# Optimization experiments

Measured on AMD Instinct MI355X. Metric: run time of the kernel, lower is better.

The kernel has to match this reference:

```python
import jax, jax.numpy as jnp
from jax import lax
import numpy as np

B, T, I, H, L, C = 64, 512, 128, 256, 2, 3


def _lstm_layer(x, W_ih, W_hh, b_ih, b_hh):
    # x: [B, T, in_dim]; W_ih: [4H, in_dim]; W_hh: [4H, H]
    # PyTorch gate order: i, f, g, o
    gates_x = jnp.einsum('bti,gi->btg', x, W_ih) + b_ih + b_hh  # [B, T, 4H]
    h0 = jnp.zeros((x.shape[0], W_hh.shape[1]), x.dtype)
    c0 = h0

    def step(carry, gx):
        h, c = carry
        g = gx + h @ W_hh.T  # [B, 4H]
        i, f, gg, o = jnp.split(g, 4, axis=-1)
        i = jax.nn.sigmoid(i)
        f = jax.nn.sigmoid(f)
        gg = jnp.tanh(gg)
        o = jax.nn.sigmoid(o)
        c = f * c + i * gg
        h = o * jnp.tanh(c)
        return (h, c), h

    _, hs = lax.scan(step, (h0, c0), jnp.swapaxes(gates_x, 0, 1))  # [T, B, H]
    return jnp.swapaxes(hs, 0, 1)  # [B, T, H]


def setup_inputs() -> dict:
    key = jax.random.key(0)
    ks = jax.random.split(key, 12)
    s = 1.0 / np.sqrt(H)
    u = lambda k, shape: jax.random.uniform(k, shape, jnp.float32, -s, s)
    return {
        'x': jax.random.normal(ks[0], (B, T, I), jnp.float32),
        'W_ih_0': u(ks[1], (4 * H, I)),
        'W_hh_0': u(ks[2], (4 * H, H)),
        'b_ih_0': u(ks[3], (4 * H,)),
        'b_hh_0': u(ks[4], (4 * H,)),
        'W_ih_1': u(ks[5], (4 * H, H)),
        'W_hh_1': u(ks[6], (4 * H, H)),
        'b_ih_1': u(ks[7], (4 * H,)),
        'b_hh_1': u(ks[8], (4 * H,)),
        'fc_w': u(ks[9], (C, H)),
        'fc_b': u(ks[10], (C,)),
    }


def reference(x, W_ih_0, W_hh_0, b_ih_0, b_hh_0, W_ih_1, W_hh_1, b_ih_1, b_hh_1, fc_w, fc_b):
    h = _lstm_layer(x, W_ih_0, W_hh_0, b_ih_0, b_hh_0)
    h = _lstm_layer(h, W_ih_1, W_hh_1, b_ih_1, b_hh_1)
    last = h[:, -1, :]                      # [B, H]
    logits = last @ fc_w.T + fc_b           # [B, C]
    return jax.nn.softmax(logits, axis=1)
```

## Files before the change

### kernel.cpp

```cpp
#include <hip/hip_runtime.h>
#include <cstdint>
#include <cstddef>

typedef _Float16 half2_t __attribute__((ext_vector_type(2)));
typedef _Float16 half8_t __attribute__((ext_vector_type(8)));
typedef float f32x4 __attribute__((ext_vector_type(4)));

static __device__ __forceinline__ float fdot2(half2_t a, half2_t b, float c) {
    return __builtin_amdgcn_fdot2(a, b, c, false);
}
static __device__ __forceinline__ half2_t h2(unsigned int u) {
    return __builtin_bit_cast(half2_t, u);
}
static __device__ __forceinline__ float sigm(float x) {
    return 1.f / (1.f + __expf(-x));
}
static __device__ __forceinline__ float tanh_fast(float x) {
    float ax = fabsf(x);
    float e = __expf(2.f * ax);
    float r = 1.f - 2.f / (e + 1.f);
    return copysignf(r, x);
}

__global__ __launch_bounds__(256) void prep_whh(const float* __restrict__ Whh,
                                                const float* __restrict__ bih,
                                                const float* __restrict__ bhh,
                                                uint4* __restrict__ Wp,
                                                float* __restrict__ bias) {
    int n = blockIdx.x * 256 + threadIdx.x;
    if (n < 1024) bias[n] = bih[n] + bhh[n];
    int p = n >> 9;
    int idx = n & 511;
    int qq = idx >> 8, jj = idx & 255;
    int g = p >> 4, u = p & 15;
    int row = g * 256 + jj;
    int kb = qq * 128 + u * 8;
    union { uint4 u4; _Float16 h[8]; } cv;
#pragma unroll
    for (int i = 0; i < 8; ++i) cv.h[i] = (_Float16)Whh[row * 256 + kb + i];
    Wp[p * 512 + idx] = cv.u4;
}

__global__ __launch_bounds__(256) void cvt_f16(const float* __restrict__ in,
                                               _Float16* __restrict__ out, int n4) {
    int i = blockIdx.x * 256 + threadIdx.x;
    if (i < n4) {
        float4 v = ((const float4*)in)[i];
        union { ushort4 u; _Float16 h[4]; } cv;
        cv.h[0] = (_Float16)v.x; cv.h[1] = (_Float16)v.y;
        cv.h[2] = (_Float16)v.z; cv.h[3] = (_Float16)v.w;
        ((ushort4*)out)[i] = cv.u;
    }
}

__global__ __launch_bounds__(256) void gemm_mfma(const _Float16* __restrict__ A,
                                                 const _Float16* __restrict__ Bw,
                                                 const float* __restrict__ bias,
                                                 float* __restrict__ Cmat, int K) {
    __shared__ _Float16 As[64][72];
    __shared__ _Float16 Bs[64][72];
    const int tid = threadIdx.x;
    const int wave = tid >> 6, lane = tid & 63;
    const int quad = lane >> 4, l16 = lane & 15;
    const int m0 = blockIdx.x * 64, n0 = blockIdx.y * 64;
    const int sr = tid >> 2;
    const int sc = (tid & 3) * 16;

    f32x4 acc[4] = {};

    for (int k0 = 0; k0 < K; k0 += 64) {
        const uint4 a0v = *(const uint4*)(A + (size_t)(m0 + sr) * K + k0 + sc);
        const uint4 a1v = *(const uint4*)(A + (size_t)(m0 + sr) * K + k0 + sc + 8);
        const uint4 b0v = *(const uint4*)(Bw + (size_t)(n0 + sr) * K + k0 + sc);
        const uint4 b1v = *(const uint4*)(Bw + (size_t)(n0 + sr) * K + k0 + sc + 8);
        __syncthreads();
        *(uint4*)&As[sr][sc] = a0v;
        *(uint4*)&As[sr][sc + 8] = a1v;
        *(uint4*)&Bs[sr][sc] = b0v;
        *(uint4*)&Bs[sr][sc + 8] = b1v;
        __syncthreads();
#pragma unroll
        for (int kc = 0; kc < 64; kc += 32) {
            half8_t af = *(const half8_t*)&As[wave * 16 + l16][kc + quad * 8];
#pragma unroll
            for (int nb = 0; nb < 4; ++nb) {
                half8_t bf = *(const half8_t*)&Bs[nb * 16 + l16][kc + quad * 8];
                acc[nb] = __builtin_amdgcn_mfma_f32_16x16x32_f16(af, bf, acc[nb], 0, 0, 0);
            }
        }
    }
#pragma unroll
    for (int nb = 0; nb < 4; ++nb) {
#pragma unroll
        for (int i = 0; i < 4; ++i) {
            int row = m0 + wave * 16 + quad * 4 + i;
            int col = n0 + nb * 16 + l16;
            Cmat[(size_t)row * 1024 + col] = acc[nb][i] + bias[col];
        }
    }
}

__global__ __launch_bounds__(512, 2)
void lstm_scan(const float* __restrict__ gx,
               const uint4* __restrict__ Wp,
               _Float16* __restrict__ h_out,
               int store_all) {
    const int b = blockIdx.x;
    const int tid = threadIdx.x;
    const int q = tid >> 8;
    const int j = tid & 255;
    const int l = tid & 63;

    __shared__ uint4 wlds[16 * 512];
    __shared__ f32x4 pex[512] __attribute__((aligned(16)));
    __shared__ _Float16 hbuf[2][256] __attribute__((aligned(16)));
    __shared__ _Float16 hist[8][256] __attribute__((aligned(16)));

#pragma unroll
    for (int p = 0; p < 16; ++p) wlds[p * 512 + tid] = Wp[(48 + p) * 512 + tid];
    uint4 wreg[48];
#pragma unroll
    for (int p = 0; p < 48; ++p) wreg[p] = Wp[p * 512 + tid];

    if (tid < 256) hbuf[0][tid] = (_Float16)0.f;
    float c = 0.f;
    const float* gxb = gx + (size_t)b * 512 * 1024 + (size_t)(q * 512 + j);
    float gA = gxb[0], gB = gxb[256];
    __syncthreads();

    for (int t = 0; t < 512; ++t) {
        float gA_n = 0.f, gB_n = 0.f;
        if (t < 511) {
            gA_n = gxb[(size_t)(t + 1) * 1024];
            gB_n = gxb[(size_t)(t + 1) * 1024 + 256];
        }

        const char* hpB = (const char*)&hbuf[t & 1][0] + q * 256;
        const uint4 hv4 = *(const uint4*)(hpB + (l & 15) * 16);

        float a0 = 0.f, a1 = 0.f, a2 = 0.f, a3 = 0.f;
#pragma unroll
        for (int u = 0; u < 16; ++u) {
            const unsigned hx = (unsigned)__builtin_amdgcn_readlane((int)hv4.x, u);
            const unsigned hy = (unsigned)__builtin_amdgcn_readlane((int)hv4.y, u);
            const unsigned hz = (unsigned)__builtin_amdgcn_readlane((int)hv4.z, u);
            const unsigned hw = (unsigned)__builtin_amdgcn_readlane((int)hv4.w, u);
            const uint4 w0 = wreg[u];
            const uint4 w1 = wreg[16 + u];
            const uint4 w2 = wreg[32 + u];
            const uint4 w3 = wlds[u * 512 + tid];
            a0 = fdot2(h2(w0.x), h2(hx), a0);
            a1 = fdot2(h2(w1.x), h2(hx), a1);
            a2 = fdot2(h2(w2.x), h2(hx), a2);
            a3 = fdot2(h2(w3.x), h2(hx), a3);
            a0 = fdot2(h2(w0.y), h2(hy), a0);
            a1 = fdot2(h2(w1.y), h2(hy), a1);
            a2 = fdot2(h2(w2.y), h2(hy), a2);
            a3 = fdot2(h2(w3.y), h2(hy), a3);
            a0 = fdot2(h2(w0.z), h2(hz), a0);
            a1 = fdot2(h2(w1.z), h2(hz), a1);
            a2 = fdot2(h2(w2.z), h2(hz), a2);
            a3 = fdot2(h2(w3.z), h2(hz), a3);
            a0 = fdot2(h2(w0.w), h2(hw), a0);
            a1 = fdot2(h2(w1.w), h2(hw), a1);
            a2 = fdot2(h2(w2.w), h2(hw), a2);
            a3 = fdot2(h2(w3.w), h2(hw), a3);
        }
        if (q == 0) { a0 += gA; a1 += gB; }
        else        { a2 += gA; a3 += gB; }

        f32x4 pv = {a0, a1, a2, a3};
        pex[tid] = pv;
        gA = gA_n; gB = gB_n;
        __syncthreads();

        if (tid < 256) {
            const f32x4 v0 = pex[tid];
            const f32x4 v1 = pex[256 + tid];
            const float ai = v0[0] + v1[0];
            const float af = v0[1] + v1[1];
            const float ag = v0[2] + v1[2];
            const float ao = v0[3] + v1[3];
            const float iv = sigm(ai);
            const float fv = sigm(af);
            const float gv = tanh_fast(ag);
            const float ov = sigm(ao);
            c = fv * c + iv * gv;
            const _Float16 hh = (_Float16)(ov * tanh_fast(c));
            hbuf[(t + 1) & 1][tid] = hh;
            if (store_all) hist[t & 7][tid] = hh;
        }
        __syncthreads();

        if (store_all && (t & 7) == 7) {
            const uint2 v = ((const uint2*)hist)[tid];
            *(uint2*)(h_out + (size_t)b * 512 * 256 + (size_t)(t - 7) * 256 + tid * 4) = v;
        }
    }
    if (!store_all && tid < 256) {
        h_out[(size_t)b * 256 + tid] = hbuf[0][tid];
    }
}

__global__ __launch_bounds__(64) void fc_softmax(const _Float16* __restrict__ hlast,
                                                 const float* __restrict__ fcw,
                                                 const float* __restrict__ fcb,
                                                 float* __restrict__ out) {
    const int b = blockIdx.x;
    const int lane = threadIdx.x;
    const _Float16* h = hlast + (size_t)b * 256;
    float p0 = 0.f, p1 = 0.f, p2 = 0.f;
    for (int k = lane; k < 256; k += 64) {
        float hv = (float)h[k];
        p0 += hv * fcw[k];
        p1 += hv * fcw[256 + k];
        p2 += hv * fcw[512 + k];
    }
#pragma unroll
    for (int off = 32; off > 0; off >>= 1) {
        p0 += __shfl_down(p0, off);
        p1 += __shfl_down(p1, off);
        p2 += __shfl_down(p2, off);
    }
    if (lane == 0) {
        float l0 = p0 + fcb[0], l1 = p1 + fcb[1], l2 = p2 + fcb[2];
        float m = fmaxf(l0, fmaxf(l1, l2));
        float e0 = __expf(l0 - m), e1 = __expf(l1 - m), e2 = __expf(l2 - m);
        float s = 1.f / (e0 + e1 + e2);
        out[b * 3 + 0] = e0 * s;
        out[b * 3 + 1] = e1 * s;
        out[b * 3 + 2] = e2 * s;
    }
}

extern "C" void kernel_launch(void* const* d_in, const int* in_sizes, int n_in,
                              void* d_out, int out_size, void* d_ws, size_t ws_size,
                              hipStream_t stream) {
    const float* x    = (const float*)d_in[0];
    const float* Wih0 = (const float*)d_in[1];
    const float* Whh0 = (const float*)d_in[2];
    const float* bih0 = (const float*)d_in[3];
    const float* bhh0 = (const float*)d_in[4];
    const float* Wih1 = (const float*)d_in[5];
    const float* Whh1 = (const float*)d_in[6];
    const float* bih1 = (const float*)d_in[7];
    const float* bhh1 = (const float*)d_in[8];
    const float* fcw  = (const float*)d_in[9];
    const float* fcb  = (const float*)d_in[10];
    float* out = (float*)d_out;

    char* ws = (char*)d_ws;
    float* gx        = (float*)ws;     ws += (size_t)32768 * 1024 * 4;
    _Float16* h0f    = (_Float16*)ws;  ws += (size_t)32768 * 256 * 2;
    _Float16* xh     = (_Float16*)ws;  ws += (size_t)32768 * 128 * 2;
    _Float16* hlast  = (_Float16*)ws;  ws += (size_t)64 * 256 * 2;
    _Float16* Wih0h  = (_Float16*)ws;  ws += (size_t)1024 * 128 * 2;
    _Float16* Wih1h  = (_Float16*)ws;  ws += (size_t)1024 * 256 * 2;
    uint4* Wp0       = (uint4*)ws;     ws += (size_t)1024 * 256 * 2;
    uint4* Wp1       = (uint4*)ws;     ws += (size_t)1024 * 256 * 2;
    float* bias0     = (float*)ws;     ws += 4096;
    float* bias1     = (float*)ws;     ws += 4096;

    prep_whh<<<128, 256, 0, stream>>>(Whh0, bih0, bhh0, Wp0, bias0);
    prep_whh<<<128, 256, 0, stream>>>(Whh1, bih1, bhh1, Wp1, bias1);
    cvt_f16<<<4096, 256, 0, stream>>>(x, xh, 32768 * 128 / 4);
    cvt_f16<<<128, 256, 0, stream>>>(Wih0, Wih0h, 1024 * 128 / 4);
    cvt_f16<<<256, 256, 0, stream>>>(Wih1, Wih1h, 1024 * 256 / 4);

    gemm_mfma<<<dim3(512, 16), 256, 0, stream>>>(xh, Wih0h, bias0, gx, 128);
    lstm_scan<<<64, 512, 0, stream>>>(gx, Wp0, h0f, 1);

    gemm_mfma<<<dim3(512, 16), 256, 0, stream>>>(h0f, Wih1h, bias1, gx, 256);
    lstm_scan<<<64, 512, 0, stream>>>(gx, Wp1, hlast, 0);

    fc_softmax<<<64, 64, 0, stream>>>(hlast, fcw, fcb, out);
}
```

Before: 1.829 ms.

## Broadcast hidden state via scalar loads from global ring buffer instead of LDS readlane

The recurrent hidden state now goes to a per-block 64-slot global ring buffer instead of LDS. Each step reads it back with s_dcache_inv plus s_load_dwordx16 into SGPRs, which replaces 64 v_readlane ops per step with scalar operands. The LDS-resident weight slice is software-prefetched two iterations ahead. The design relies on global writes becoming visible to the scalar cache after vmcnt(0) and a barrier. That puts a global-memory round trip on the serial critical path and carries a coherence risk.

```diff
diff --git a/kernel.cpp b/kernel.cpp
--- a/kernel.cpp
+++ b/kernel.cpp
@@ -5,6 +5,7 @@
 typedef _Float16 half2_t __attribute__((ext_vector_type(2)));
 typedef _Float16 half8_t __attribute__((ext_vector_type(8)));
 typedef float f32x4 __attribute__((ext_vector_type(4)));
+typedef int i16v __attribute__((ext_vector_type(16)));
 
 static __device__ __forceinline__ float fdot2(half2_t a, half2_t b, float c) {
     return __builtin_amdgcn_fdot2(a, b, c, false);
@@ -103,17 +104,16 @@
 __global__ __launch_bounds__(512, 2)
 void lstm_scan(const float* __restrict__ gx,
                const uint4* __restrict__ Wp,
+               _Float16* __restrict__ stg,
                _Float16* __restrict__ h_out,
                int store_all) {
     const int b = blockIdx.x;
     const int tid = threadIdx.x;
     const int q = tid >> 8;
     const int j = tid & 255;
-    const int l = tid & 63;
 
     __shared__ uint4 wlds[16 * 512];
     __shared__ f32x4 pex[512] __attribute__((aligned(16)));
-    __shared__ _Float16 hbuf[2][256] __attribute__((aligned(16)));
     __shared__ _Float16 hist[8][256] __attribute__((aligned(16)));
 
 #pragma unroll
@@ -122,33 +122,64 @@
 #pragma unroll
     for (int p = 0; p < 48; ++p) wreg[p] = Wp[p * 512 + tid];
 
-    if (tid < 256) hbuf[0][tid] = (_Float16)0.f;
+    _Float16* stw = stg + (size_t)b * 64 * 256;
+    if (tid < 256) stw[j] = (_Float16)0.f;
     float c = 0.f;
+    _Float16 last_h = (_Float16)0.f;
     const float* gxb = gx + (size_t)b * 512 * 1024 + (size_t)(q * 512 + j);
     float gA = gxb[0], gB = gxb[256];
+    const uint64_t stbu = (uint64_t)(uintptr_t)((const char*)stw + (size_t)q * 256);
+    const uint32_t stb_lo = (uint32_t)__builtin_amdgcn_readfirstlane((int)(uint32_t)stbu);
+    const uint32_t stb_hi = (uint32_t)__builtin_amdgcn_readfirstlane((int)(uint32_t)(stbu >> 32));
     __syncthreads();
 
     for (int t = 0; t < 512; ++t) {
+        const uint64_t spa = (((uint64_t)stb_hi << 32) | stb_lo)
+                             + (uint64_t)((t & 63) * 512);
+        i16v ha, hb, hc, hd;
+        asm volatile("s_dcache_inv" ::: "memory");
+        asm volatile("s_load_dwordx16 %0, %2, 0x0\n\t"
+                     "s_load_dwordx16 %1, %2, 0x40"
+                     : "=&s"(ha), "=&s"(hb) : "s"(spa) : "memory");
+
         float gA_n = 0.f, gB_n = 0.f;
         if (t < 511) {
             gA_n = gxb[(size_t)(t + 1) * 1024];
             gB_n = gxb[(size_t)(t + 1) * 1024 + 256];
         }
-
-        const char* hpB = (const char*)&hbuf[t & 1][0] + q * 256;
-        const uint4 hv4 = *(const uint4*)(hpB + (l & 15) * 16);
+        asm volatile("s_waitcnt lgkmcnt(0)" ::: "memory");
+
+        uint4 w3_p[2];
+        w3_p[0] = wlds[0 * 512 + tid];
+        w3_p[1] = wlds[1 * 512 + tid];
 
         float a0 = 0.f, a1 = 0.f, a2 = 0.f, a3 = 0.f;
 #pragma unroll
         for (int u = 0; u < 16; ++u) {
-            const unsigned hx = (unsigned)__builtin_amdgcn_readlane((int)hv4.x, u);
-            const unsigned hy = (unsigned)__builtin_amdgcn_readlane((int)hv4.y, u);
-            const unsigned hz = (unsigned)__builtin_amdgcn_readlane((int)hv4.z, u);
-            const unsigned hw = (unsigned)__builtin_amdgcn_readlane((int)hv4.w, u);
+            if (u == 8) {
+                asm volatile("s_load_dwordx16 %0, %2, 0x80\n\t"
+                             "s_load_dwordx16 %1, %2, 0xC0"
+                             : "=&s"(hc), "=&s"(hd) : "s"(spa) : "memory");
+                asm volatile("s_waitcnt lgkmcnt(0)" ::: "memory");
+            }
+            const uint4 w3 = w3_p[u & 1];
+            if (u < 14) w3_p[u & 1] = wlds[(u + 2) * 512 + tid];
             const uint4 w0 = wreg[u];
             const uint4 w1 = wreg[16 + u];
             const uint4 w2 = wreg[32 + u];
-            const uint4 w3 = wlds[u * 512 + tid];
+            const int d = u * 4;
+            const unsigned hx = (unsigned)(d < 16 ? ha[d]
+                                 : d < 32 ? hb[d - 16]
+                                 : d < 48 ? hc[d - 32] : hd[d - 48]);
+            const unsigned hy = (unsigned)(d + 1 < 16 ? ha[d + 1]
+                                 : d + 1 < 32 ? hb[d - 15]
+                                 : d + 1 < 48 ? hc[d - 31] : hd[d - 47]);
+            const unsigned hz = (unsigned)(d + 2 < 16 ? ha[d + 2]
+                                 : d + 2 < 32 ? hb[d - 14]
+                                 : d + 2 < 48 ? hc[d - 30] : hd[d - 46]);
+            const unsigned hw = (unsigned)(d + 3 < 16 ? ha[d + 3]
+                                 : d + 3 < 32 ? hb[d - 13]
+                                 : d + 3 < 48 ? hc[d - 29] : hd[d - 45]);
             a0 = fdot2(h2(w0.x), h2(hx), a0);
             a1 = fdot2(h2(w1.x), h2(hx), a1);
             a2 = fdot2(h2(w2.x), h2(hx), a2);
@@ -172,7 +203,9 @@
         f32x4 pv = {a0, a1, a2, a3};
         pex[tid] = pv;
         gA = gA_n; gB = gB_n;
-        __syncthreads();
+        asm volatile("s_waitcnt lgkmcnt(0)" ::: "memory");
+        __builtin_amdgcn_s_barrier();
+        asm volatile("" ::: "memory");
 
         if (tid < 256) {
             const f32x4 v0 = pex[tid];
@@ -187,10 +220,13 @@
             const float ov = sigm(ao);
             c = fv * c + iv * gv;
             const _Float16 hh = (_Float16)(ov * tanh_fast(c));
-            hbuf[(t + 1) & 1][tid] = hh;
-            if (store_all) hist[t & 7][tid] = hh;
-        }
-        __syncthreads();
+            stw[(size_t)((t + 1) & 63) * 256 + j] = hh;
+            last_h = hh;
+            if (store_all) hist[t & 7][j] = hh;
+        }
+        asm volatile("s_waitcnt vmcnt(0) lgkmcnt(0)" ::: "memory");
+        __builtin_amdgcn_s_barrier();
+        asm volatile("" ::: "memory");
 
         if (store_all && (t & 7) == 7) {
             const uint2 v = ((const uint2*)hist)[tid];
@@ -198,7 +234,7 @@
         }
     }
     if (!store_all && tid < 256) {
-        h_out[(size_t)b * 256 + tid] = hbuf[0][tid];
+        h_out[(size_t)b * 256 + tid] = last_h;
     }
 }
 
@@ -260,6 +296,7 @@
     uint4* Wp1       = (uint4*)ws;     ws += (size_t)1024 * 256 * 2;
     float* bias0     = (float*)ws;     ws += 4096;
     float* bias1     = (float*)ws;     ws += 4096;
+    _Float16* stg    = (_Float16*)ws;  ws += (size_t)64 * 64 * 256 * 2;
 
     prep_whh<<<128, 256, 0, stream>>>(Whh0, bih0, bhh0, Wp0, bias0);
     prep_whh<<<128, 256, 0, stream>>>(Whh1, bih1, bhh1, Wp1, bias1);
@@ -268,10 +305,10 @@
     cvt_f16<<<256, 256, 0, stream>>>(Wih1, Wih1h, 1024 * 256 / 4);
 
     gemm_mfma<<<dim3(512, 16), 256, 0, stream>>>(xh, Wih0h, bias0, gx, 128);
-    lstm_scan<<<64, 512, 0, stream>>>(gx, Wp0, h0f, 1);
+    lstm_scan<<<64, 512, 0, stream>>>(gx, Wp0, stg, h0f, 1);
 
     gemm_mfma<<<dim3(512, 16), 256, 0, stream>>>(h0f, Wih1h, bias1, gx, 256);
-    lstm_scan<<<64, 512, 0, stream>>>(gx, Wp1, hlast, 0);
+    lstm_scan<<<64, 512, 0, stream>>>(gx, Wp1, stg, hlast, 0);
 
     fc_softmax<<<64, 64, 0, stream>>>(hlast, fcw, fcb, out);
 }
```

Measured after the change: 1.893 ms. +3.5%, slower.
